# Performance work log

Hardware: AMD Instinct MI355X
Metric: run time of the kernel (lower is better)

## Reference

```python
import jax, jax.numpy as jnp
import numpy as np

PAD_TOKEN = 0

def setup_inputs() -> dict:
    key = jax.random.key(0)
    ks = jax.random.split(key, 6)
    B, S, E, W, V = 16, 2048, 128, 128, 7
    x = jax.random.randint(ks[0], (B, S), 0, V, dtype=jnp.int64)
    emb_table = jax.random.normal(ks[1], (V, E), dtype=jnp.float32)
    fc_w = jax.random.normal(ks[2], (E, W * E), dtype=jnp.float32) * 0.02
    fc_b = jax.random.normal(ks[3], (E,), dtype=jnp.float32) * 0.02
    out_w = jax.random.normal(ks[4], (1, E), dtype=jnp.float32) * 0.02
    out_b = jax.random.normal(ks[5], (1,), dtype=jnp.float32) * 0.02
    return {"x": x, "emb_table": emb_table, "fc_w": fc_w, "fc_b": fc_b,
            "out_w": out_w, "out_b": out_b}

def reference(x, emb_table, fc_w, fc_b, out_w, out_b):
    B, S = x.shape
    V, E = emb_table.shape
    Eo, WE = fc_w.shape
    W = WE // E
    # embedding lookup: [B, S, E]
    ex = emb_table[x]
    # causal left pad by W-1 along seq -> [B, S+W-1, E]
    padded = jnp.pad(ex, ((0, 0), (W - 1, 0), (0, 0)))
    # torch unfold gives windows[b,s,e,k] = padded[b, s+k, e], flattened index e*W + k.
    # Equivalent implicit conv: kernel[k, e, o] = fc_w[o, e*W + k]  (WIO layout)
    kernel = jnp.transpose(fc_w.reshape(Eo, E, W), (2, 1, 0))
    conv = jax.lax.conv_general_dilated(
        padded, kernel, window_strides=(1,), padding='VALID',
        dimension_numbers=('NWC', 'WIO', 'NWC'))  # [B, S, Eo]
    h = conv + fc_b
    # output_layer: Linear(E -> 1), then squeeze -> [B, S]
    logits = jnp.einsum('bse,oe->bso', h, out_w)[..., 0] + out_b[0]
    # return_last_seq=True: gather at last non-pad count index
    last_idx = jnp.sum(x != PAD_TOKEN, axis=-1) - 1  # [B]
    out = logits[jnp.arange(B), last_idx].reshape(-1, 1)
    return out
```

## Files before the change

### kernel.cpp

```cpp
#include <hip/hip_runtime.h>

#define BB 16
#define SS 2048
#define EE 128
#define WW 128
#define VV 7
#define WE (WW * EE)

__global__ __launch_bounds__(256) void k1_slice(const int* __restrict__ x,
                                                const float* __restrict__ emb,
                                                const float* __restrict__ fc_w,
                                                const float* __restrict__ out_w,
                                                float* __restrict__ part) {
    __shared__ float red[16][64];
    __shared__ float v[64];
    __shared__ float embS[8];
    __shared__ int lastS[BB];

    const int c = blockIdx.x;
    const int t = threadIdx.x;
    const int lane = t & 63;
    const int w = t >> 6;
    const int e = c >> 1;
    const int k0 = (c & 1) * 64;

    const int oo = lane >> 4;
    const int kq = lane & 15;
    const float* fbase = fc_w + (size_t)e * WW + k0 + kq * 4;
    float4 f[8];
    float ow[8];
#pragma unroll
    for (int it = 0; it < 8; ++it) {
        const int o = w * 32 + it * 4 + oo;
        f[it] = *reinterpret_cast<const float4*>(fbase + (size_t)o * WE);
        ow[it] = out_w[o];
    }

    if (t >= 64 && t < 72) {
        const int tok = t - 64;
        embS[tok] = (tok < VV) ? emb[tok * EE + e] : 0.f;
    }

    const int bt = t >> 4;
    const int ch = t & 15;
    const int4* xq = reinterpret_cast<const int4*>(x);
    int cnt = 0;
#pragma unroll
    for (int i = 0; i < 32; ++i) {
        const int4 q = xq[bt * 512 + i * 16 + ch];
        cnt += (q.x != 0) + (q.y != 0) + (q.z != 0) + (q.w != 0);
    }
#pragma unroll
    for (int off = 8; off; off >>= 1) cnt += __shfl_down(cnt, off, 16);
    if (ch == 0) lastS[bt] = cnt - 1;

    float4 acc = make_float4(0.f, 0.f, 0.f, 0.f);
#pragma unroll
    for (int it = 0; it < 8; ++it) {
        acc.x += ow[it] * f[it].x;
        acc.y += ow[it] * f[it].y;
        acc.z += ow[it] * f[it].z;
        acc.w += ow[it] * f[it].w;
    }
    *reinterpret_cast<float4*>(&red[w * 4 + oo][kq * 4]) = acc;
    __syncthreads();
    if (t < 64) {
        float s = 0.f;
#pragma unroll
        for (int g = 0; g < 16; ++g) s += red[g][t];
        v[t] = s;
    }
    __syncthreads();

    const int b = t >> 4;
    const int kg = t & 15;
    const int last = lastS[b];
    const int* xb = x + b * SS;
    float val = 0.f;
#pragma unroll
    for (int q2 = 0; q2 < 4; ++q2) {
        const int k = k0 + kg * 4 + q2;
        const int j = last - (WW - 1) + k;
        const int tok = (j >= 0) ? xb[j] : VV;
        val += v[kg * 4 + q2] * embS[tok];
    }
#pragma unroll
    for (int off = 8; off; off >>= 1) val += __shfl_down(val, off, 16);
    if (kg == 0) part[c * 16 + b] = val;
}

__global__ __launch_bounds__(256) void k2_reduce(const float* __restrict__ part,
                                                 const float* __restrict__ fc_b,
                                                 const float* __restrict__ out_w,
                                                 const float* __restrict__ out_b,
                                                 float* __restrict__ out) {
    __shared__ float mat[16][17];
    __shared__ float bred[2];

    const int t = threadIdx.x;
    const int lane = t & 63;
    const int w = t >> 6;

    float p = (t < EE) ? out_w[t] * fc_b[t] : 0.f;
#pragma unroll
    for (int off = 32; off; off >>= 1) p += __shfl_down(p, off, 64);
    if (lane == 0 && w < 2) bred[w] = p;

    const int g = t >> 4;
    const int b = t & 15;
    float s = 0.f;
#pragma unroll
    for (int i = 0; i < 16; ++i)
        s += part[(g * 16 + i) * 16 + b];
    mat[g][b] = s;
    __syncthreads();
    if (t < BB) {
        float tot = bred[0] + bred[1] + out_b[0];
#pragma unroll
        for (int gg = 0; gg < 16; ++gg) tot += mat[gg][t];
        out[t] = tot;
    }
}

extern "C" void kernel_launch(void* const* d_in, const int* in_sizes, int n_in,
                              void* d_out, int out_size, void* d_ws, size_t ws_size,
                              hipStream_t stream) {
    const int* x = (const int*)d_in[0];
    const float* emb = (const float*)d_in[1];
    const float* fc_w = (const float*)d_in[2];
    const float* fc_b = (const float*)d_in[3];
    const float* out_w = (const float*)d_in[4];
    const float* out_b = (const float*)d_in[5];
    float* part = (float*)d_ws;
    float* out = (float*)d_out;

    k1_slice<<<256, 256, 0, stream>>>(x, emb, fc_w, out_w, part);
    k2_reduce<<<1, 256, 0, stream>>>(part, fc_b, out_w, out_b, out);
}
```

Measured before the change: 73.72 us.

## Move token counting out of the weight-slice kernel into a per-batch dot kernel

The first kernel now only folds out_w into fc_w and writes the 128x128 vector v to workspace. Previously every one of its 256 blocks redundantly scanned the whole token array to compute last indices. A second kernel with one block per batch row now counts non-pad tokens once, gathers the 128-token window, and dots the embeddings with v. It also folds in the bias and reduction, replacing the old partial-sum reduce kernel. The cost is a global round trip for v, and the second kernel runs only 16 blocks.

```diff
diff --git a/kernel.cpp b/kernel.cpp
--- a/kernel.cpp
+++ b/kernel.cpp
@@ -7,15 +7,10 @@
 #define VV 7
 #define WE (WW * EE)
 
-__global__ __launch_bounds__(256) void k1_slice(const int* __restrict__ x,
-                                                const float* __restrict__ emb,
-                                                const float* __restrict__ fc_w,
-                                                const float* __restrict__ out_w,
-                                                float* __restrict__ part) {
+__global__ __launch_bounds__(256) void k1_v(const float* __restrict__ fc_w,
+                                            const float* __restrict__ out_w,
+                                            float* __restrict__ v) {
     __shared__ float red[16][64];
-    __shared__ float v[64];
-    __shared__ float embS[8];
-    __shared__ int lastS[BB];
 
     const int c = blockIdx.x;
     const int t = threadIdx.x;
@@ -36,24 +31,6 @@
         ow[it] = out_w[o];
     }
 
-    if (t >= 64 && t < 72) {
-        const int tok = t - 64;
-        embS[tok] = (tok < VV) ? emb[tok * EE + e] : 0.f;
-    }
-
-    const int bt = t >> 4;
-    const int ch = t & 15;
-    const int4* xq = reinterpret_cast<const int4*>(x);
-    int cnt = 0;
-#pragma unroll
-    for (int i = 0; i < 32; ++i) {
-        const int4 q = xq[bt * 512 + i * 16 + ch];
-        cnt += (q.x != 0) + (q.y != 0) + (q.z != 0) + (q.w != 0);
-    }
-#pragma unroll
-    for (int off = 8; off; off >>= 1) cnt += __shfl_down(cnt, off, 16);
-    if (ch == 0) lastS[bt] = cnt - 1;
-
     float4 acc = make_float4(0.f, 0.f, 0.f, 0.f);
 #pragma unroll
     for (int it = 0; it < 8; ++it) {
@@ -64,62 +41,79 @@
     }
     *reinterpret_cast<float4*>(&red[w * 4 + oo][kq * 4]) = acc;
     __syncthreads();
+
     if (t < 64) {
         float s = 0.f;
 #pragma unroll
         for (int g = 0; g < 16; ++g) s += red[g][t];
-        v[t] = s;
+        v[(size_t)e * WW + k0 + t] = s;
+    }
+}
+
+__global__ __launch_bounds__(256) void k2_dot(const int* __restrict__ x,
+                                              const float* __restrict__ emb,
+                                              const float* __restrict__ v,
+                                              const float* __restrict__ fc_b,
+                                              const float* __restrict__ out_w,
+                                              const float* __restrict__ out_b,
+                                              float* __restrict__ out) {
+    __shared__ float embS[8 * EE];
+    __shared__ int winTok[WW];
+    __shared__ int cntW[4];
+    __shared__ float wsum[4];
+
+    const int b = blockIdx.x;
+    const int t = threadIdx.x;
+    const int lane = t & 63;
+    const int w = t >> 6;
+    const int* xb = x + b * SS;
+
+    {
+        const int f0 = t * 4;
+#pragma unroll
+        for (int j = 0; j < 4; ++j) {
+            const int fi = f0 + j;
+            embS[fi] = (fi < VV * EE) ? emb[fi] : 0.f;
+        }
+    }
+
+    const int4* xq = reinterpret_cast<const int4*>(xb);
+    const int4 q0 = xq[t * 2];
+    const int4 q1 = xq[t * 2 + 1];
+    int cnt = (q0.x != 0) + (q0.y != 0) + (q0.z != 0) + (q0.w != 0)
+            + (q1.x != 0) + (q1.y != 0) + (q1.z != 0) + (q1.w != 0);
+#pragma unroll
+    for (int off = 32; off; off >>= 1) cnt += __shfl_down(cnt, off);
+    if (lane == 0) cntW[w] = cnt;
+    __syncthreads();
+    const int last = cntW[0] + cntW[1] + cntW[2] + cntW[3] - 1;
+
+    if (t < WW) {
+        const int j = last - (WW - 1) + t;
+        winTok[t] = (j >= 0) ? xb[j] : VV;
     }
     __syncthreads();
 
-    const int b = t >> 4;
-    const int kg = t & 15;
-    const int last = lastS[b];
-    const int* xb = x + b * SS;
-    float val = 0.f;
+    float val = (t < EE) ? out_w[t] * fc_b[t] : 0.f;
+
+    const int e = t >> 1;
+    const int kh = t & 1;
+    const float4* vb4 = reinterpret_cast<const float4*>(v + e * WW + kh * 64);
+    const int* wt = winTok + kh * 64;
 #pragma unroll
-    for (int q2 = 0; q2 < 4; ++q2) {
-        const int k = k0 + kg * 4 + q2;
-        const int j = last - (WW - 1) + k;
-        const int tok = (j >= 0) ? xb[j] : VV;
-        val += v[kg * 4 + q2] * embS[tok];
+    for (int k4 = 0; k4 < 16; ++k4) {
+        const float4 vv = vb4[k4];
+        val += embS[wt[k4 * 4 + 0] * EE + e] * vv.x;
+        val += embS[wt[k4 * 4 + 1] * EE + e] * vv.y;
+        val += embS[wt[k4 * 4 + 2] * EE + e] * vv.z;
+        val += embS[wt[k4 * 4 + 3] * EE + e] * vv.w;
     }
+
 #pragma unroll
-    for (int off = 8; off; off >>= 1) val += __shfl_down(val, off, 16);
-    if (kg == 0) part[c * 16 + b] = val;
-}
-
-__global__ __launch_bounds__(256) void k2_reduce(const float* __restrict__ part,
-                                                 const float* __restrict__ fc_b,
-                                                 const float* __restrict__ out_w,
-                                                 const float* __restrict__ out_b,
-                                                 float* __restrict__ out) {
-    __shared__ float mat[16][17];
-    __shared__ float bred[2];
-
-    const int t = threadIdx.x;
-    const int lane = t & 63;
-    const int w = t >> 6;
-
-    float p = (t < EE) ? out_w[t] * fc_b[t] : 0.f;
-#pragma unroll
-    for (int off = 32; off; off >>= 1) p += __shfl_down(p, off, 64);
-    if (lane == 0 && w < 2) bred[w] = p;
-
-    const int g = t >> 4;
-    const int b = t & 15;
-    float s = 0.f;
-#pragma unroll
-    for (int i = 0; i < 16; ++i)
-        s += part[(g * 16 + i) * 16 + b];
-    mat[g][b] = s;
+    for (int off = 32; off; off >>= 1) val += __shfl_down(val, off);
+    if (lane == 0) wsum[w] = val;
     __syncthreads();
-    if (t < BB) {
-        float tot = bred[0] + bred[1] + out_b[0];
-#pragma unroll
-        for (int gg = 0; gg < 16; ++gg) tot += mat[gg][t];
-        out[t] = tot;
-    }
+    if (t == 0) out[b] = wsum[0] + wsum[1] + wsum[2] + wsum[3] + out_b[0];
 }
 
 extern "C" void kernel_launch(void* const* d_in, const int* in_sizes, int n_in,
@@ -131,9 +125,9 @@
     const float* fc_b = (const float*)d_in[3];
     const float* out_w = (const float*)d_in[4];
     const float* out_b = (const float*)d_in[5];
-    float* part = (float*)d_ws;
+    float* v = (float*)d_ws;
     float* out = (float*)d_out;
 
-    k1_slice<<<256, 256, 0, stream>>>(x, emb, fc_w, out_w, part);
-    k2_reduce<<<1, 256, 0, stream>>>(part, fc_b, out_w, out_b, out);
+    k1_v<<<256, 256, 0, stream>>>(fc_w, out_w, v);
+    k2_dot<<<16, 256, 0, stream>>>(x, emb, v, fc_b, out_w, out_b, out);
 }
```

Measured after the change: 74.74 us. About the same (+1.4%).
